# Performance work log

Hardware: AMD Instinct MI355X
Metric: run time of the kernel (lower is better)

## Reference

```python
import jax, jax.numpy as jnp
import numpy as np

DEPTH = 4
HEADS = 8
DIM = 512
HIDDEN = int(DIM * 2.0)  # mlp_ratio=2.0
K_HOPS = 4
EPS = 1e-5


def _layer_norm(x, g, b):
    m = jnp.mean(x, axis=-1, keepdims=True)
    v = jnp.mean(jnp.square(x - m), axis=-1, keepdims=True)
    return (x - m) * jax.lax.rsqrt(v + EPS) * g + b


def setup_inputs() -> dict:
    key = jax.random.key(0)
    ks = jax.random.split(key, 20)
    B, N, C = 2048, 17, DIM
    inp = {
        "x": jax.random.normal(ks[0], (B, N, C), jnp.float32),
        "Hstack": jax.random.uniform(ks[1], (K_HOPS, N, N), jnp.float32),
        "hop_logits_attn": jax.random.normal(ks[2], (HEADS, K_HOPS), jnp.float32),
        "rel_alpha": jax.random.normal(ks[3], (HEADS,), jnp.float32),
        # per-layer params stacked over depth
        "qkv_w": jax.random.normal(ks[4], (DEPTH, 3 * C, C), jnp.float32) * 0.02,
        "qkv_b": jnp.zeros((DEPTH, 3 * C), jnp.float32),
        "proj_w": jax.random.normal(ks[5], (DEPTH, C, C), jnp.float32) * 0.02,
        "proj_b": jnp.zeros((DEPTH, C), jnp.float32),
        "ln1_g": jnp.ones((DEPTH, C), jnp.float32),
        "ln1_b": jnp.zeros((DEPTH, C), jnp.float32),
        "ln2_g": jnp.ones((DEPTH, C), jnp.float32),
        "ln2_b": jnp.zeros((DEPTH, C), jnp.float32),
        "fc1_w": jax.random.normal(ks[6], (DEPTH, HIDDEN, C), jnp.float32) * 0.02,
        "fc1_b": jnp.zeros((DEPTH, HIDDEN), jnp.float32),
        "fc2_w": jax.random.normal(ks[7], (DEPTH, C, HIDDEN), jnp.float32) * 0.02,
        "fc2_b": jnp.zeros((DEPTH, C), jnp.float32),
    }
    return inp


def _block(x, Hstack, hop_logits_attn, rel_alpha, qkv_w, qkv_b, proj_w, proj_b,
           ln1_g, ln1_b, ln2_g, ln2_b, fc1_w, fc1_b, fc2_w, fc2_b):
    B, N, C = x.shape
    hd = C // HEADS
    scale = hd ** (-0.5)
    h = _layer_norm(x, ln1_g, ln1_b)
    qkv = h @ qkv_w.T + qkv_b  # [B,N,3C]
    qkv = qkv.reshape(B, N, 3, HEADS, hd).transpose(2, 0, 3, 1, 4)
    q, k, v = qkv[0], qkv[1], qkv[2]  # [B,H,N,hd]
    logits = jnp.einsum('bhnd,bhmd->bhnm', q, k) * scale
    # hop-based additive bias: softmax over hops, mixed into per-head bias
    w = jax.nn.softmax(hop_logits_attn, axis=-1)  # [H,K]
    B_head = jnp.einsum('hk,kij->hij', w, Hstack)  # [H,N,N]
    bias = rel_alpha[:, None, None] * B_head
    logits = logits + bias[None]
    attn = jax.nn.softmax(logits, axis=-1)
    out = jnp.einsum('bhnm,bhmd->bhnd', attn, v)
    out = out.transpose(0, 2, 1, 3).reshape(B, N, C)
    out = out @ proj_w.T + proj_b
    x = x + out
    h2 = _layer_norm(x, ln2_g, ln2_b)
    h2 = jax.nn.gelu(h2 @ fc1_w.T + fc1_b, approximate=False)
    x = x + (h2 @ fc2_w.T + fc2_b)
    return x


def reference(x, Hstack, hop_logits_attn, rel_alpha, qkv_w, qkv_b, proj_w, proj_b,
              ln1_g, ln1_b, ln2_g, ln2_b, fc1_w, fc1_b, fc2_w, fc2_b):
    for d in range(DEPTH):
        x = _block(x, Hstack, hop_logits_attn, rel_alpha,
                   qkv_w[d], qkv_b[d], proj_w[d], proj_b[d],
                   ln1_g[d], ln1_b[d], ln2_g[d], ln2_b[d],
                   fc1_w[d], fc1_b[d], fc2_w[d], fc2_b[d])
    return x
```

## Files before the change

### kernel.cpp

```cpp
#include <hip/hip_runtime.h>

#define DEPTHL 4
#define NHEADS 8
#define DIMC 512
#define HIDDENC 1024
#define NTOK 17
#define NROWS (2048*NTOK)

typedef __attribute__((ext_vector_type(8))) short s8v;
typedef __attribute__((ext_vector_type(4))) float f4v;
typedef __attribute__((ext_vector_type(4))) short s4v;

static __device__ __forceinline__ float bf2f(short s) {
  unsigned u = ((unsigned)(unsigned short)s) << 16;
  return __builtin_bit_cast(float, u);
}
static __device__ __forceinline__ short f2bf(float f) {
  unsigned u = __builtin_bit_cast(unsigned, f);
  u += 0x7fffu + ((u >> 16) & 1u);
  return (short)(u >> 16);
}

static __device__ __forceinline__ void load_lds16(const void* g, void* l) {
  __builtin_amdgcn_global_load_lds(
      (const __attribute__((address_space(1))) unsigned int*)g,
      (__attribute__((address_space(3))) unsigned int*)l, 16, 0, 0);
}

#define BARX() asm volatile("s_barrier" ::: "memory")
#define VMC0() asm volatile("s_waitcnt vmcnt(0)" ::: "memory")

__global__ __launch_bounds__(256) void f2bf_kernel(const float* __restrict__ in,
                                                   short* __restrict__ out, int n4) {
  int i = blockIdx.x * 256 + threadIdx.x;
  if (i < n4) {
    float4 v = ((const float4*)in)[i];
    s4v o;
    o[0] = f2bf(v.x); o[1] = f2bf(v.y); o[2] = f2bf(v.z); o[3] = f2bf(v.w);
    ((s4v*)out)[i] = o;
  }
}

__global__ __launch_bounds__(256) void ln_kernel(const float* __restrict__ x,
    const float* __restrict__ g, const float* __restrict__ b,
    short* __restrict__ h) {
  int row = blockIdx.x * 4 + (threadIdx.x >> 6);
  int lane = threadIdx.x & 63;
  const float* xr = x + (size_t)row * DIMC + lane * 8;
  float4 v0 = *(const float4*)xr;
  float4 v1 = *(const float4*)(xr + 4);
  float s = v0.x + v0.y + v0.z + v0.w + v1.x + v1.y + v1.z + v1.w;
  #pragma unroll
  for (int o = 32; o > 0; o >>= 1) s += __shfl_xor(s, o, 64);
  float mean = s * (1.0f / 512.0f);
  float d0 = v0.x-mean, d1 = v0.y-mean, d2 = v0.z-mean, d3 = v0.w-mean;
  float d4 = v1.x-mean, d5 = v1.y-mean, d6 = v1.z-mean, d7 = v1.w-mean;
  float vs = d0*d0+d1*d1+d2*d2+d3*d3+d4*d4+d5*d5+d6*d6+d7*d7;
  #pragma unroll
  for (int o = 32; o > 0; o >>= 1) vs += __shfl_xor(vs, o, 64);
  float rstd = rsqrtf(vs * (1.0f / 512.0f) + 1e-5f);
  const float* gp = g + lane * 8;
  const float* bp = b + lane * 8;
  float4 g0 = *(const float4*)gp, g1 = *(const float4*)(gp + 4);
  float4 b0 = *(const float4*)bp, b1 = *(const float4*)(bp + 4);
  s8v o;
  o[0] = f2bf(d0 * rstd * g0.x + b0.x);
  o[1] = f2bf(d1 * rstd * g0.y + b0.y);
  o[2] = f2bf(d2 * rstd * g0.z + b0.z);
  o[3] = f2bf(d3 * rstd * g0.w + b0.w);
  o[4] = f2bf(d4 * rstd * g1.x + b1.x);
  o[5] = f2bf(d5 * rstd * g1.y + b1.y);
  o[6] = f2bf(d6 * rstd * g1.z + b1.z);
  o[7] = f2bf(d7 * rstd * g1.w + b1.w);
  *(s8v*)(h + (size_t)row * DIMC + lane * 8) = o;
}

enum { EPI_BF16 = 0, EPI_RES_F32 = 1, EPI_GELU_BF16 = 2 };

template<int K, int EPI>
__global__ __launch_bounds__(256) void gemm2p(
    const short* __restrict__ A, const short* __restrict__ Bm,
    const float* __restrict__ bias, const float* __restrict__ res,
    void* __restrict__ outp, int N, int nbx) {
  constexpr int NT = K / 64;
  __shared__ __align__(16) short SA[2][8192];
  __shared__ __align__(16) short SB[2][8192];
  const int tid = threadIdx.x;
  const int wave = tid >> 6, lane = tid & 63;
  const int l15 = lane & 15, l4 = lane >> 4;
  const int nwg = gridDim.x, bid = blockIdx.x;
  const int swz = (bid & 7) * (nwg >> 3) + (bid >> 3);
  const int bx = swz % nbx, by = swz / nbx;
  const int m0 = by * 128, n0 = bx * 128;
  const int wr = wave >> 1, wc = wave & 1;

  f4v acc[4][4] = {};

  auto stageT = [&](const short* __restrict__ mat, int row0, int k0, short* ldsb) {
    #pragma unroll
    for (int q = 0; q < 4; ++q) {
      const int r = q * 32 + (tid >> 3), c = tid & 7;
      const short* src = mat + (size_t)(row0 + r) * K + k0 + ((c ^ (r & 7)) << 3);
      load_lds16(src, ldsb + q * 2048 + ((tid & ~63) << 3));
    }
  };

  stageT(A, m0, 0, SA[0]);
  stageT(Bm, n0, 0, SB[0]);
  VMC0();
  BARX();

  #pragma unroll
  for (int t = 0; t < NT; ++t) {
    const int cur = t & 1;
    if (t + 1 < NT) {
      stageT(A, m0, (t + 1) * 64, SA[cur ^ 1]);
      stageT(Bm, n0, (t + 1) * 64, SB[cur ^ 1]);
    }
    #pragma unroll
    for (int kk = 0; kk < 2; ++kk) {
      s8v af[4], bfr[4];
      #pragma unroll
      for (int i = 0; i < 4; ++i) {
        const int Ra = wr * 64 + i * 16 + l15;
        af[i] = *(const s8v*)&SA[cur][(Ra << 6) + (((kk * 4 + l4) ^ (Ra & 7)) << 3)];
        const int Rb = wc * 64 + i * 16 + l15;
        bfr[i] = *(const s8v*)&SB[cur][(Rb << 6) + (((kk * 4 + l4) ^ (Rb & 7)) << 3)];
      }
      #pragma unroll
      for (int i = 0; i < 4; ++i)
        #pragma unroll
        for (int j = 0; j < 4; ++j)
          acc[i][j] = __builtin_amdgcn_mfma_f32_16x16x32_bf16(af[i], bfr[j], acc[i][j], 0, 0, 0);
    }
    if (t + 1 < NT) VMC0();
    BARX();
  }

  const int cb = n0 + wc * 64 + l15;
  const int rb = m0 + wr * 64 + (l4 << 2);
  #pragma unroll
  for (int i = 0; i < 4; ++i) {
    #pragma unroll
    for (int j2 = 0; j2 < 4; ++j2) {
      const int n = cb + j2 * 16;
      const float bs = bias[n];
      #pragma unroll
      for (int r = 0; r < 4; ++r) {
        const int m = rb + i * 16 + r;
        const float v = acc[i][j2][r] + bs;
        const size_t off = (size_t)m * N + n;
        if constexpr (EPI == EPI_RES_F32) {
          ((float*)outp)[off] = res[off] + v;
        } else if constexpr (EPI == EPI_GELU_BF16) {
          float gv = 0.5f * v * (1.0f + erff(v * 0.70710678118654752f));
          ((short*)outp)[off] = f2bf(gv);
        } else {
          ((short*)outp)[off] = f2bf(v);
        }
      }
    }
  }
}

__global__ __launch_bounds__(256) void attnbias_kernel(const float* __restrict__ H,
    const float* __restrict__ hop_logits, const float* __restrict__ rel_alpha,
    float* __restrict__ battn) {
  int t = threadIdx.x;
  for (int e = t; e < NHEADS * NTOK * NTOK; e += 256) {
    int h = e / (NTOK * NTOK);
    int nm = e - h * NTOK * NTOK;
    float l0 = hop_logits[h * 4 + 0], l1 = hop_logits[h * 4 + 1];
    float l2 = hop_logits[h * 4 + 2], l3 = hop_logits[h * 4 + 3];
    float mx = fmaxf(fmaxf(l0, l1), fmaxf(l2, l3));
    float e0 = expf(l0 - mx), e1 = expf(l1 - mx), e2 = expf(l2 - mx), e3 = expf(l3 - mx);
    float inv = 1.0f / (e0 + e1 + e2 + e3);
    float bsum = (e0 * H[0 * 289 + nm] + e1 * H[1 * 289 + nm] +
                  e2 * H[2 * 289 + nm] + e3 * H[3 * 289 + nm]) * inv;
    battn[e] = rel_alpha[h] * bsum;
  }
}

__global__ __launch_bounds__(256) void attn_kernel(const short* __restrict__ qkv,
    const float* __restrict__ battn, short* __restrict__ out) {
  __shared__ __align__(16) short sq[4][NTOK * 64];
  __shared__ __align__(16) short sk[4][NTOK * 64];
  __shared__ __align__(16) short sv[4][NTOK * 64];
  __shared__ float sp[4][NTOK * 18];
  int w = threadIdx.x >> 6, lane = threadIdx.x & 63;
  int wid = blockIdx.x * 4 + w;
  int b = wid >> 3, h = wid & 7;

  for (int s = lane; s < NTOK * 8; s += 64) {
    int n = s >> 3, c8 = (s & 7) * 8;
    const short* rowp = qkv + (size_t)(b * NTOK + n) * 1536 + h * 64 + c8;
    *(s8v*)&sq[w][s * 8] = *(const s8v*)&rowp[0];
    *(s8v*)&sk[w][s * 8] = *(const s8v*)&rowp[512];
    *(s8v*)&sv[w][s * 8] = *(const s8v*)&rowp[1024];
  }
  __syncthreads();

  #pragma unroll
  for (int idx = 0; idx < 5; ++idx) {
    int e = idx * 64 + lane;
    int ec = e < 289 ? e : 288;
    int n = ec / 17, m = ec - n * 17;
    float acc = 0.f;
    #pragma unroll
    for (int c = 0; c < 8; ++c) {
      s8v qv = *(const s8v*)&sq[w][n * 64 + c * 8];
      s8v kv = *(const s8v*)&sk[w][m * 64 + c * 8];
      #pragma unroll
      for (int t = 0; t < 8; ++t) acc += bf2f(qv[t]) * bf2f(kv[t]);
    }
    if (e < 289) sp[w][n * 18 + m] = acc * 0.125f + battn[h * 289 + e];
  }
  __syncthreads();

  if (lane < NTOK) {
    float mx = -1e30f;
    #pragma unroll
    for (int m = 0; m < NTOK; ++m) mx = fmaxf(mx, sp[w][lane * 18 + m]);
    float pv[NTOK];
    float ssum = 0.f;
    #pragma unroll
    for (int m = 0; m < NTOK; ++m) { float ev = expf(sp[w][lane * 18 + m] - mx); pv[m] = ev; ssum += ev; }
    float inv = 1.0f / ssum;
    #pragma unroll
    for (int m = 0; m < NTOK; ++m) sp[w][lane * 18 + m] = pv[m] * inv;
  }
  __syncthreads();

  #pragma unroll
  for (int n = 0; n < NTOK; ++n) {
    float ov = 0.f;
    #pragma unroll
    for (int m = 0; m < NTOK; ++m) ov += sp[w][n * 18 + m] * bf2f(sv[w][m * 64 + lane]);
    out[(size_t)(b * NTOK + n) * DIMC + h * 64 + lane] = f2bf(ov);
  }
}

extern "C" void kernel_launch(void* const* d_in, const int* in_sizes, int n_in,
                              void* d_out, int out_size, void* d_ws, size_t ws_size,
                              hipStream_t stream) {
  const float* x_in       = (const float*)d_in[0];
  const float* Hstack     = (const float*)d_in[1];
  const float* hop_logits = (const float*)d_in[2];
  const float* rel_alpha  = (const float*)d_in[3];
  const float* qkv_w  = (const float*)d_in[4];
  const float* qkv_b  = (const float*)d_in[5];
  const float* proj_w = (const float*)d_in[6];
  const float* proj_b = (const float*)d_in[7];
  const float* ln1_g  = (const float*)d_in[8];
  const float* ln1_b  = (const float*)d_in[9];
  const float* ln2_g  = (const float*)d_in[10];
  const float* ln2_b  = (const float*)d_in[11];
  const float* fc1_w  = (const float*)d_in[12];
  const float* fc1_b  = (const float*)d_in[13];
  const float* fc2_w  = (const float*)d_in[14];
  const float* fc2_b  = (const float*)d_in[15];
  float* xout = (float*)d_out;

  short* wqkv  = (short*)d_ws;
  short* wproj = wqkv  + (size_t)4 * 1536 * 512;
  short* wfc1  = wproj + (size_t)4 * 512 * 512;
  short* wfc2  = wfc1  + (size_t)4 * 1024 * 512;
  float* battn = (float*)(wfc2 + (size_t)4 * 512 * 1024);
  short* hbuf   = (short*)(battn + 2432);
  short* qkvbuf = hbuf + (size_t)NROWS * 512;

  {
    int n4;
    n4 = 4 * 1536 * 512 / 4;
    f2bf_kernel<<<dim3((n4 + 255) / 256), dim3(256), 0, stream>>>(qkv_w, wqkv, n4);
    n4 = 4 * 512 * 512 / 4;
    f2bf_kernel<<<dim3((n4 + 255) / 256), dim3(256), 0, stream>>>(proj_w, wproj, n4);
    n4 = 4 * 1024 * 512 / 4;
    f2bf_kernel<<<dim3((n4 + 255) / 256), dim3(256), 0, stream>>>(fc1_w, wfc1, n4);
    n4 = 4 * 512 * 1024 / 4;
    f2bf_kernel<<<dim3((n4 + 255) / 256), dim3(256), 0, stream>>>(fc2_w, wfc2, n4);
  }
  attnbias_kernel<<<dim3(1), dim3(256), 0, stream>>>(Hstack, hop_logits, rel_alpha, battn);

  const int LNBLK = NROWS / 4;
  const dim3 B256(256);
  const int MB = NROWS / 128;

  for (int d = 0; d < DEPTHL; ++d) {
    const float* xres = (d == 0) ? x_in : xout;
    ln_kernel<<<dim3(LNBLK), B256, 0, stream>>>(xres, ln1_g + d * 512, ln1_b + d * 512, hbuf);
    gemm2p<512, EPI_BF16><<<dim3((1536 / 128) * MB), B256, 0, stream>>>(
        hbuf, wqkv + (size_t)d * 1536 * 512, qkv_b + d * 1536, nullptr, qkvbuf, 1536, 1536 / 128);
    attn_kernel<<<dim3(2048 * NHEADS / 4), B256, 0, stream>>>(qkvbuf, battn, hbuf);
    gemm2p<512, EPI_RES_F32><<<dim3((512 / 128) * MB), B256, 0, stream>>>(
        hbuf, wproj + (size_t)d * 512 * 512, proj_b + d * 512, xres, xout, 512, 512 / 128);
    ln_kernel<<<dim3(LNBLK), B256, 0, stream>>>(xout, ln2_g + d * 512, ln2_b + d * 512, hbuf);
    gemm2p<512, EPI_GELU_BF16><<<dim3((1024 / 128) * MB), B256, 0, stream>>>(
        hbuf, wfc1 + (size_t)d * 1024 * 512, fc1_b + d * 1024, nullptr, qkvbuf, 1024, 1024 / 128);
    gemm2p<1024, EPI_RES_F32><<<dim3((512 / 128) * MB), B256, 0, stream>>>(
        qkvbuf, wfc2 + (size_t)d * 512 * 1024, fc2_b + d * 512, xout, xout, 512, 512 / 128);
  }
}
```

Baseline: 1.831 ms.

## Keep full weight panel resident in LDS and stream activations from registers

New measurement: 2.620 ms. 43.0% more time.

```diff
diff --git a/kernel.cpp b/kernel.cpp
--- a/kernel.cpp
+++ b/kernel.cpp
@@ -77,86 +77,87 @@
 
 enum { EPI_BF16 = 0, EPI_RES_F32 = 1, EPI_GELU_BF16 = 2 };
 
-template<int K, int EPI>
-__global__ __launch_bounds__(256) void gemm2p(
+template<int K, int NP, int EPI>
+__global__ __launch_bounds__(512) void gemm_ws(
     const short* __restrict__ A, const short* __restrict__ Bm,
     const float* __restrict__ bias, const float* __restrict__ res,
     void* __restrict__ outp, int N, int nbx) {
   constexpr int NT = K / 64;
-  __shared__ __align__(16) short SA[2][8192];
-  __shared__ __align__(16) short SB[2][8192];
+  constexpr int NK = K / 32;
+  __shared__ __align__(16) short SB[NT * 4096];
   const int tid = threadIdx.x;
   const int wave = tid >> 6, lane = tid & 63;
   const int l15 = lane & 15, l4 = lane >> 4;
   const int nwg = gridDim.x, bid = blockIdx.x;
   const int swz = (bid & 7) * (nwg >> 3) + (bid >> 3);
   const int bx = swz % nbx, by = swz / nbx;
-  const int m0 = by * 128, n0 = bx * 128;
-  const int wr = wave >> 1, wc = wave & 1;
-
-  f4v acc[4][4] = {};
-
-  auto stageT = [&](const short* __restrict__ mat, int row0, int k0, short* ldsb) {
-    #pragma unroll
-    for (int q = 0; q < 4; ++q) {
-      const int r = q * 32 + (tid >> 3), c = tid & 7;
-      const short* src = mat + (size_t)(row0 + r) * K + k0 + ((c ^ (r & 7)) << 3);
-      load_lds16(src, ldsb + q * 2048 + ((tid & ~63) << 3));
-    }
-  };
-
-  stageT(A, m0, 0, SA[0]);
-  stageT(Bm, n0, 0, SB[0]);
-  VMC0();
-  BARX();
-
-  #pragma unroll
-  for (int t = 0; t < NT; ++t) {
-    const int cur = t & 1;
-    if (t + 1 < NT) {
-      stageT(A, m0, (t + 1) * 64, SA[cur ^ 1]);
-      stageT(Bm, n0, (t + 1) * 64, SB[cur ^ 1]);
-    }
-    #pragma unroll
-    for (int kk = 0; kk < 2; ++kk) {
-      s8v af[4], bfr[4];
+  const int n0 = bx * 64;
+
+  {
+    const int r = tid >> 3, c = tid & 7;
+    const short* src0 = Bm + (size_t)(n0 + r) * K + ((c ^ (r & 7)) << 3);
+    #pragma unroll
+    for (int t = 0; t < NT; ++t)
+      load_lds16(src0 + t * 64, &SB[t * 4096 + ((tid & ~63) << 3)]);
+    VMC0();
+    BARX();
+  }
+
+  const int arow = wave * 64 + l15;
+  const int acol = l4 * 8;
+
+  #pragma unroll
+  for (int p = 0; p < NP; ++p) {
+    const int m0 = (by * NP + p) * 512;
+    const short* Ab = A + (size_t)(m0 + arow) * K + acol;
+    f4v acc[4][4] = {};
+    s8v a[3][4];
+    #pragma unroll
+    for (int rt = 0; rt < 4; ++rt) a[0][rt] = *(const s8v*)(Ab + (size_t)rt * 16 * K);
+    #pragma unroll
+    for (int rt = 0; rt < 4; ++rt) a[1][rt] = *(const s8v*)(Ab + (size_t)rt * 16 * K + 32);
+
+    #pragma unroll
+    for (int ks = 0; ks < NK; ++ks) {
+      if (ks + 2 < NK) {
+        #pragma unroll
+        for (int rt = 0; rt < 4; ++rt)
+          a[(ks + 2) % 3][rt] = *(const s8v*)(Ab + (size_t)rt * 16 * K + (ks + 2) * 32);
+      }
+      s8v bf[4];
       #pragma unroll
-      for (int i = 0; i < 4; ++i) {
-        const int Ra = wr * 64 + i * 16 + l15;
-        af[i] = *(const s8v*)&SA[cur][(Ra << 6) + (((kk * 4 + l4) ^ (Ra & 7)) << 3)];
-        const int Rb = wc * 64 + i * 16 + l15;
-        bfr[i] = *(const s8v*)&SB[cur][(Rb << 6) + (((kk * 4 + l4) ^ (Rb & 7)) << 3)];
+      for (int ct = 0; ct < 4; ++ct) {
+        const int nl = ct * 16 + l15;
+        const int cc = (ks & 1) * 4 + l4;
+        bf[ct] = *(const s8v*)&SB[(ks >> 1) * 4096 + (nl << 6) + ((cc ^ (nl & 7)) << 3)];
       }
       #pragma unroll
-      for (int i = 0; i < 4; ++i)
+      for (int rt = 0; rt < 4; ++rt)
         #pragma unroll
-        for (int j = 0; j < 4; ++j)
-          acc[i][j] = __builtin_amdgcn_mfma_f32_16x16x32_bf16(af[i], bfr[j], acc[i][j], 0, 0, 0);
+        for (int ct = 0; ct < 4; ++ct)
+          acc[rt][ct] = __builtin_amdgcn_mfma_f32_16x16x32_bf16(a[ks % 3][rt], bf[ct], acc[rt][ct], 0, 0, 0);
     }
-    if (t + 1 < NT) VMC0();
-    BARX();
-  }
-
-  const int cb = n0 + wc * 64 + l15;
-  const int rb = m0 + wr * 64 + (l4 << 2);
-  #pragma unroll
-  for (int i = 0; i < 4; ++i) {
-    #pragma unroll
-    for (int j2 = 0; j2 < 4; ++j2) {
-      const int n = cb + j2 * 16;
-      const float bs = bias[n];
+
+    const int rbase = m0 + wave * 64 + (l4 << 2);
+    #pragma unroll
+    for (int rt = 0; rt < 4; ++rt) {
       #pragma unroll
-      for (int r = 0; r < 4; ++r) {
-        const int m = rb + i * 16 + r;
-        const float v = acc[i][j2][r] + bs;
-        const size_t off = (size_t)m * N + n;
-        if constexpr (EPI == EPI_RES_F32) {
-          ((float*)outp)[off] = res[off] + v;
-        } else if constexpr (EPI == EPI_GELU_BF16) {
-          float gv = 0.5f * v * (1.0f + erff(v * 0.70710678118654752f));
-          ((short*)outp)[off] = f2bf(gv);
-        } else {
-          ((short*)outp)[off] = f2bf(v);
+      for (int ct = 0; ct < 4; ++ct) {
+        const int n = n0 + ct * 16 + l15;
+        const float bs = bias[n];
+        #pragma unroll
+        for (int r = 0; r < 4; ++r) {
+          const int m = rbase + rt * 16 + r;
+          const float v = acc[rt][ct][r] + bs;
+          const size_t off = (size_t)m * N + n;
+          if constexpr (EPI == EPI_RES_F32) {
+            ((float*)outp)[off] = res[off] + v;
+          } else if constexpr (EPI == EPI_GELU_BF16) {
+            float gv = 0.5f * v * (1.0f + erff(v * 0.70710678118654752f));
+            ((short*)outp)[off] = f2bf(gv);
+          } else {
+            ((short*)outp)[off] = f2bf(v);
+          }
         }
       }
     }
@@ -283,21 +284,20 @@
   attnbias_kernel<<<dim3(1), dim3(256), 0, stream>>>(Hstack, hop_logits, rel_alpha, battn);
 
   const int LNBLK = NROWS / 4;
-  const dim3 B256(256);
-  const int MB = NROWS / 128;
+  const dim3 B256(256), B512(512);
 
   for (int d = 0; d < DEPTHL; ++d) {
     const float* xres = (d == 0) ? x_in : xout;
     ln_kernel<<<dim3(LNBLK), B256, 0, stream>>>(xres, ln1_g + d * 512, ln1_b + d * 512, hbuf);
-    gemm2p<512, EPI_BF16><<<dim3((1536 / 128) * MB), B256, 0, stream>>>(
-        hbuf, wqkv + (size_t)d * 1536 * 512, qkv_b + d * 1536, nullptr, qkvbuf, 1536, 1536 / 128);
+    gemm_ws<512, 2, EPI_BF16><<<dim3(24 * 34), B512, 0, stream>>>(
+        hbuf, wqkv + (size_t)d * 1536 * 512, qkv_b + d * 1536, nullptr, qkvbuf, 1536, 24);
     attn_kernel<<<dim3(2048 * NHEADS / 4), B256, 0, stream>>>(qkvbuf, battn, hbuf);
-    gemm2p<512, EPI_RES_F32><<<dim3((512 / 128) * MB), B256, 0, stream>>>(
-        hbuf, wproj + (size_t)d * 512 * 512, proj_b + d * 512, xres, xout, 512, 512 / 128);
+    gemm_ws<512, 1, EPI_RES_F32><<<dim3(8 * 68), B512, 0, stream>>>(
+        hbuf, wproj + (size_t)d * 512 * 512, proj_b + d * 512, xres, xout, 512, 8);
     ln_kernel<<<dim3(LNBLK), B256, 0, stream>>>(xout, ln2_g + d * 512, ln2_b + d * 512, hbuf);
-    gemm2p<512, EPI_GELU_BF16><<<dim3((1024 / 128) * MB), B256, 0, stream>>>(
-        hbuf, wfc1 + (size_t)d * 1024 * 512, fc1_b + d * 1024, nullptr, qkvbuf, 1024, 1024 / 128);
-    gemm2p<1024, EPI_RES_F32><<<dim3((512 / 128) * MB), B256, 0, stream>>>(
-        qkvbuf, wfc2 + (size_t)d * 512 * 1024, fc2_b + d * 512, xout, xout, 512, 512 / 128);
-  }
-}
+    gemm_ws<512, 2, EPI_GELU_BF16><<<dim3(16 * 34), B512, 0, stream>>>(
+        hbuf, wfc1 + (size_t)d * 1024 * 512, fc1_b + d * 1024, nullptr, qkvbuf, 1024, 16);
+    gemm_ws<1024, 1, EPI_RES_F32><<<dim3(8 * 68), B512, 0, stream>>>(
+        qkvbuf, wfc2 + (size_t)d * 512 * 1024, fc2_b + d * 512, xout, xout, 512, 8);
+  }
+}
```

## Use four-stage LDS pipeline with K=32 tiles in GEMM kernel

Applied to the files above, without the earlier changes.

After: 1.662 ms. -9.3%, faster.

```diff
diff --git a/kernel.cpp b/kernel.cpp
--- a/kernel.cpp
+++ b/kernel.cpp
@@ -28,7 +28,7 @@
 }
 
 #define BARX() asm volatile("s_barrier" ::: "memory")
-#define VMC0() asm volatile("s_waitcnt vmcnt(0)" ::: "memory")
+#define VMC(n) asm volatile("s_waitcnt vmcnt(" #n ")" ::: "memory")
 
 __global__ __launch_bounds__(256) void f2bf_kernel(const float* __restrict__ in,
                                                    short* __restrict__ out, int n4) {
@@ -78,13 +78,13 @@
 enum { EPI_BF16 = 0, EPI_RES_F32 = 1, EPI_GELU_BF16 = 2 };
 
 template<int K, int EPI>
-__global__ __launch_bounds__(256) void gemm2p(
+__global__ __launch_bounds__(256) void gemm_p4(
     const short* __restrict__ A, const short* __restrict__ Bm,
     const float* __restrict__ bias, const float* __restrict__ res,
     void* __restrict__ outp, int N, int nbx) {
-  constexpr int NT = K / 64;
-  __shared__ __align__(16) short SA[2][8192];
-  __shared__ __align__(16) short SB[2][8192];
+  constexpr int NT = K / 32;
+  __shared__ __align__(16) short SA[4][4096];
+  __shared__ __align__(16) short SB[4][4096];
   const int tid = threadIdx.x;
   const int wave = tid >> 6, lane = tid & 63;
   const int l15 = lane & 15, l4 = lane >> 4;
@@ -96,59 +96,59 @@
 
   f4v acc[4][4] = {};
 
-  auto stageT = [&](const short* __restrict__ mat, int row0, int k0, short* ldsb) {
-    #pragma unroll
-    for (int q = 0; q < 4; ++q) {
-      const int r = q * 32 + (tid >> 3), c = tid & 7;
-      const short* src = mat + (size_t)(row0 + r) * K + k0 + ((c ^ (r & 7)) << 3);
-      load_lds16(src, ldsb + q * 2048 + ((tid & ~63) << 3));
+  auto stage1 = [&](const short* __restrict__ mat, int row0, int k0, short* buf) {
+    #pragma unroll
+    for (int q = 0; q < 2; ++q) {
+      const int lr = q * 32 + (tid >> 3);
+      const int sl = (tid & 7) ^ (lr & 7);
+      const short* src = mat + (size_t)(row0 + lr * 2 + (sl >> 2)) * K + k0 + ((sl & 3) << 3);
+      load_lds16(src, buf + q * 2048 + ((tid & ~63) << 3));
     }
   };
-
-  stageT(A, m0, 0, SA[0]);
-  stageT(Bm, n0, 0, SB[0]);
-  VMC0();
-  BARX();
+  auto rdfrag = [&](const short* buf, int r) -> s8v {
+    const int lr = r >> 1;
+    const int sl = (((r & 1) << 2) | l4) ^ (lr & 7);
+    return *(const s8v*)&buf[lr * 64 + (sl << 3)];
+  };
+
+  stage1(A, m0, 0, SA[0]);  stage1(Bm, n0, 0, SB[0]);
+  stage1(A, m0, 32, SA[1]); stage1(Bm, n0, 32, SB[1]);
+  stage1(A, m0, 64, SA[2]); stage1(Bm, n0, 64, SB[2]);
 
   #pragma unroll
   for (int t = 0; t < NT; ++t) {
-    const int cur = t & 1;
-    if (t + 1 < NT) {
-      stageT(A, m0, (t + 1) * 64, SA[cur ^ 1]);
-      stageT(Bm, n0, (t + 1) * 64, SB[cur ^ 1]);
+    if (t + 3 < NT) {
+      stage1(A, m0, (t + 3) * 32, SA[(t + 3) & 3]);
+      stage1(Bm, n0, (t + 3) * 32, SB[(t + 3) & 3]);
     }
-    #pragma unroll
-    for (int kk = 0; kk < 2; ++kk) {
-      s8v af[4], bfr[4];
+    VMC(8);
+    BARX();
+    s8v af[4], bf[4];
+    #pragma unroll
+    for (int rt = 0; rt < 4; ++rt) af[rt] = rdfrag(SA[t & 3], wr * 64 + rt * 16 + l15);
+    #pragma unroll
+    for (int ct = 0; ct < 4; ++ct) bf[ct] = rdfrag(SB[t & 3], wc * 64 + ct * 16 + l15);
+    __builtin_amdgcn_s_setprio(1);
+    #pragma unroll
+    for (int rt = 0; rt < 4; ++rt)
       #pragma unroll
-      for (int i = 0; i < 4; ++i) {
-        const int Ra = wr * 64 + i * 16 + l15;
-        af[i] = *(const s8v*)&SA[cur][(Ra << 6) + (((kk * 4 + l4) ^ (Ra & 7)) << 3)];
-        const int Rb = wc * 64 + i * 16 + l15;
-        bfr[i] = *(const s8v*)&SB[cur][(Rb << 6) + (((kk * 4 + l4) ^ (Rb & 7)) << 3)];
-      }
-      #pragma unroll
-      for (int i = 0; i < 4; ++i)
-        #pragma unroll
-        for (int j = 0; j < 4; ++j)
-          acc[i][j] = __builtin_amdgcn_mfma_f32_16x16x32_bf16(af[i], bfr[j], acc[i][j], 0, 0, 0);
-    }
-    if (t + 1 < NT) VMC0();
+      for (int ct = 0; ct < 4; ++ct)
+        acc[rt][ct] = __builtin_amdgcn_mfma_f32_16x16x32_bf16(af[rt], bf[ct], acc[rt][ct], 0, 0, 0);
+    __builtin_amdgcn_s_setprio(0);
     BARX();
   }
 
-  const int cb = n0 + wc * 64 + l15;
-  const int rb = m0 + wr * 64 + (l4 << 2);
-  #pragma unroll
-  for (int i = 0; i < 4; ++i) {
-    #pragma unroll
-    for (int j2 = 0; j2 < 4; ++j2) {
-      const int n = cb + j2 * 16;
+  #pragma unroll
+  for (int rt = 0; rt < 4; ++rt) {
+    #pragma unroll
+    for (int ct = 0; ct < 4; ++ct) {
+      const int n = n0 + wc * 64 + ct * 16 + l15;
       const float bs = bias[n];
+      const int mb = m0 + wr * 64 + rt * 16 + (l4 << 2);
       #pragma unroll
       for (int r = 0; r < 4; ++r) {
-        const int m = rb + i * 16 + r;
-        const float v = acc[i][j2][r] + bs;
+        const int m = mb + r;
+        const float v = acc[rt][ct][r] + bs;
         const size_t off = (size_t)m * N + n;
         if constexpr (EPI == EPI_RES_F32) {
           ((float*)outp)[off] = res[off] + v;
@@ -289,15 +289,15 @@
   for (int d = 0; d < DEPTHL; ++d) {
     const float* xres = (d == 0) ? x_in : xout;
     ln_kernel<<<dim3(LNBLK), B256, 0, stream>>>(xres, ln1_g + d * 512, ln1_b + d * 512, hbuf);
-    gemm2p<512, EPI_BF16><<<dim3((1536 / 128) * MB), B256, 0, stream>>>(
-        hbuf, wqkv + (size_t)d * 1536 * 512, qkv_b + d * 1536, nullptr, qkvbuf, 1536, 1536 / 128);
+    gemm_p4<512, EPI_BF16><<<dim3(12 * MB), B256, 0, stream>>>(
+        hbuf, wqkv + (size_t)d * 1536 * 512, qkv_b + d * 1536, nullptr, qkvbuf, 1536, 12);
     attn_kernel<<<dim3(2048 * NHEADS / 4), B256, 0, stream>>>(qkvbuf, battn, hbuf);
-    gemm2p<512, EPI_RES_F32><<<dim3((512 / 128) * MB), B256, 0, stream>>>(
-        hbuf, wproj + (size_t)d * 512 * 512, proj_b + d * 512, xres, xout, 512, 512 / 128);
+    gemm_p4<512, EPI_RES_F32><<<dim3(4 * MB), B256, 0, stream>>>(
+        hbuf, wproj + (size_t)d * 512 * 512, proj_b + d * 512, xres, xout, 512, 4);
     ln_kernel<<<dim3(LNBLK), B256, 0, stream>>>(xout, ln2_g + d * 512, ln2_b + d * 512, hbuf);
-    gemm2p<512, EPI_GELU_BF16><<<dim3((1024 / 128) * MB), B256, 0, stream>>>(
-        hbuf, wfc1 + (size_t)d * 1024 * 512, fc1_b + d * 1024, nullptr, qkvbuf, 1024, 1024 / 128);
-    gemm2p<1024, EPI_RES_F32><<<dim3((512 / 128) * MB), B256, 0, stream>>>(
-        qkvbuf, wfc2 + (size_t)d * 512 * 1024, fc2_b + d * 512, xout, xout, 512, 512 / 128);
-  }
-}
+    gemm_p4<512, EPI_GELU_BF16><<<dim3(8 * MB), B256, 0, stream>>>(
+        hbuf, wfc1 + (size_t)d * 1024 * 512, fc1_b + d * 1024, nullptr, qkvbuf, 1024, 8);
+    gemm_p4<1024, EPI_RES_F32><<<dim3(4 * MB), B256, 0, stream>>>(
+        qkvbuf, wfc2 + (size_t)d * 512 * 1024, fc2_b + d * 512, xout, xout, 512, 4);
+  }
+}
```
